# Performance work log

Measured on AMD Instinct MI355X. Metric: run time of the kernel, lower is better.

Reference implementation:

```python
import jax, jax.numpy as jnp
import numpy as np

VOCAB = 50000; D = 512; H = 512; HD = H // 2; L = 2
T = 2048; NTAGS = 20; START = 18; END = 19
NEG = -10000.0


def setup_inputs() -> dict:
    key = jax.random.key(0)
    ks = jax.random.split(key, 24)
    s = 0.05
    rn = lambda k, shape: jax.random.normal(k, shape, jnp.float32) * s
    inp = {}
    inp["sentence"] = jax.random.randint(ks[0], (T,), 0, VOCAB)
    inp["emb"] = rn(ks[1], (VOCAB, D))
    i = 2
    for l in range(L):
        din = D if l == 0 else H
        for d in ("f", "b"):
            inp[f"l{l}{d}_Wih"] = rn(ks[i], (4 * HD, din)); i += 1
            inp[f"l{l}{d}_Whh"] = rn(ks[i], (4 * HD, HD)); i += 1
            inp[f"l{l}{d}_bih"] = rn(ks[i], (4 * HD,)); i += 1
            inp[f"l{l}{d}_bhh"] = rn(ks[i], (4 * HD,)); i += 1
    inp["W_out"] = rn(ks[i], (NTAGS, H)); i += 1
    inp["b_out"] = rn(ks[i], (NTAGS,)); i += 1
    tr = jax.random.normal(ks[i], (NTAGS, NTAGS), jnp.float32)
    tr = tr.at[START, :].set(NEG).at[:, END].set(NEG)
    inp["transitions"] = tr
    return inp


def _lstm_dir(x, Wih, Whh, bih, bhh, reverse):
    # x: [T, din]; precompute input contribution to all 4 gates (i,f,g,o order).
    xg = x @ Wih.T + bih  # [T, 4*HD]
    h0 = jnp.zeros((Whh.shape[1],), x.dtype)

    def step(carry, xt):
        h, c = carry
        z = xt + h @ Whh.T + bhh
        i, f, g, o = jnp.split(z, 4)
        c = jax.nn.sigmoid(f) * c + jax.nn.sigmoid(i) * jnp.tanh(g)
        h = jax.nn.sigmoid(o) * jnp.tanh(c)
        return (h, c), h

    _, hs = jax.lax.scan(step, (h0, h0), xg, reverse=reverse)
    return hs  # [T, HD], outputs aligned with timesteps in both directions


def _feats(sentence, emb, layers, W_out, b_out):
    x = emb[sentence]  # [T, D]
    for (Wf, Uf, bf, cf, Wb, Ub, bb, cb) in layers:
        hf = _lstm_dir(x, Wf, Uf, bf, cf, False)
        hb = _lstm_dir(x, Wb, Ub, bb, cb, True)
        x = jnp.concatenate([hf, hb], axis=-1)  # [T, H]
    return x @ W_out.T + b_out  # [T, NTAGS]


def _viterbi(feats, transitions):
    v0 = jnp.full((NTAGS,), NEG, feats.dtype).at[START].set(0.0)

    def step(v, feat):
        scores = v[None, :] + transitions  # [next_tag, prev_tag]
        bp = jnp.argmax(scores, axis=1)
        v_new = jnp.max(scores, axis=1) + feat
        return v_new, bp

    v_last, bps = jax.lax.scan(step, v0, feats)  # bps: [T, NTAGS]
    terminal = v_last + transitions[END]
    best = jnp.argmax(terminal)
    score = terminal[best]

    def back(tag, bp):
        return bp[tag], tag  # emit tag at this timestep, move to its predecessor

    _, path = jax.lax.scan(back, best, bps, reverse=True)
    return score, path


def reference(sentence, emb, l0f_Wih, l0f_Whh, l0f_bih, l0f_bhh, l0b_Wih, l0b_Whh, l0b_bih, l0b_bhh, l1f_Wih, l1f_Whh, l1f_bih, l1f_bhh, l1b_Wih, l1b_Whh, l1b_bih, l1b_bhh, W_out, b_out, transitions):
    layers = [
        (l0f_Wih, l0f_Whh, l0f_bih, l0f_bhh, l0b_Wih, l0b_Whh, l0b_bih, l0b_bhh),
        (l1f_Wih, l1f_Whh, l1f_bih, l1f_bhh, l1b_Wih, l1b_Whh, l1b_bih, l1b_bhh),
    ]
    feats = _feats(sentence, emb, layers, W_out, b_out)
    return _viterbi(feats, transitions)
```

## Files before the change

kernel.cpp:

```cpp
#include <hip/hip_runtime.h>
#include <math.h>


#define T_LEN 2048
#define DMODEL 512
#define HD 256
#define NTAGS 20
#define START_TAG 18
#define END_TAG 19
#define NCAND 64

__device__ __forceinline__ float fsig(float x) {
  return 1.0f / (1.0f + __expf(-x));
}
__device__ __forceinline__ float ftanh(float x) {
  float xc = fminf(15.0f, fmaxf(-15.0f, x));
  float e = __expf(2.0f * xc);
  return (e - 1.0f) / (e + 1.0f);
}

__device__ __forceinline__ unsigned long long rd_l2(unsigned long long* p) {
  unsigned long long old;
  unsigned long long zero = 0;
  asm volatile("global_atomic_add_x2 %0, %1, %2, off sc0\n\ts_waitcnt vmcnt(0)"
               : "=&v"(old)
               : "v"(p), "v"(zero)
               : "memory");
  return old;
}
__device__ __forceinline__ void pub_l2(unsigned long long* p,
                                       unsigned long long v) {
  *(volatile unsigned long long*)p = v;
}

__global__ void embed_k(const int* __restrict__ sent,
                        const float* __restrict__ emb,
                        float* __restrict__ x0) {
  int t = blockIdx.x;
  int tid = threadIdx.x;
  int tok = sent[t];
  const float4* src = (const float4*)(emb + (size_t)tok * DMODEL);
  float4* dst = (float4*)(x0 + (size_t)t * DMODEL);
  dst[tid] = src[tid];
}

__global__ __launch_bounds__(256) void gemm_xg_k(
    const float* __restrict__ X,
    const float* __restrict__ Wf, const float* __restrict__ Wb,
    const float* __restrict__ bf, const float* __restrict__ bb,
    float* __restrict__ outf, float* __restrict__ outb) {
  int bx = blockIdx.x;
  int by = blockIdx.y;
  int dir = blockIdx.z;
  const float* W = dir ? Wb : Wf;
  const float* bias = dir ? bb : bf;
  float* out = dir ? outb : outf;

  __shared__ __align__(16) float Xs[16][132];
  __shared__ __align__(16) float Ws[16][132];

  int tid = threadIdx.x;
  int tx = tid & 15;
  int ty = tid >> 4;

  float acc[8][8];
#pragma unroll
  for (int i = 0; i < 8; i++)
#pragma unroll
    for (int j = 0; j < 8; j++) acc[i][j] = 0.0f;

  for (int kt = 0; kt < DMODEL / 16; kt++) {
    __syncthreads();
#pragma unroll
    for (int l = 0; l < 2; l++) {
      int fi = tid + l * 256;
      int row = fi >> 2;
      int kq = fi & 3;
      float4 xv = *(const float4*)(X + (size_t)(by * 128 + row) * DMODEL + kt * 16 + kq * 4);
      Xs[kq * 4 + 0][row] = xv.x;
      Xs[kq * 4 + 1][row] = xv.y;
      Xs[kq * 4 + 2][row] = xv.z;
      Xs[kq * 4 + 3][row] = xv.w;
      float4 wv = *(const float4*)(W + (size_t)(bx * 128 + row) * DMODEL + kt * 16 + kq * 4);
      Ws[kq * 4 + 0][row] = wv.x;
      Ws[kq * 4 + 1][row] = wv.y;
      Ws[kq * 4 + 2][row] = wv.z;
      Ws[kq * 4 + 3][row] = wv.w;
    }
    __syncthreads();
#pragma unroll
    for (int k = 0; k < 16; k++) {
      float4 a0 = *(const float4*)&Xs[k][ty * 4];
      float4 a1 = *(const float4*)&Xs[k][64 + ty * 4];
      float4 b0 = *(const float4*)&Ws[k][tx * 4];
      float4 b1 = *(const float4*)&Ws[k][64 + tx * 4];
      float a[8] = {a0.x, a0.y, a0.z, a0.w, a1.x, a1.y, a1.z, a1.w};
      float b[8] = {b0.x, b0.y, b0.z, b0.w, b1.x, b1.y, b1.z, b1.w};
#pragma unroll
      for (int i = 0; i < 8; i++)
#pragma unroll
        for (int j = 0; j < 8; j++) acc[i][j] += a[i] * b[j];
    }
  }

  float4 bv0 = *(const float4*)(bias + bx * 128 + tx * 4);
  float4 bv1 = *(const float4*)(bias + bx * 128 + 64 + tx * 4);
  float bb8[8] = {bv0.x, bv0.y, bv0.z, bv0.w, bv1.x, bv1.y, bv1.z, bv1.w};
#pragma unroll
  for (int i = 0; i < 8; i++) {
    int row = by * 128 + ((i < 4) ? (ty * 4 + i) : (64 + ty * 4 + (i - 4)));
    float4 o0 = {acc[i][0] + bb8[0], acc[i][1] + bb8[1], acc[i][2] + bb8[2], acc[i][3] + bb8[3]};
    float4 o1 = {acc[i][4] + bb8[4], acc[i][5] + bb8[5], acc[i][6] + bb8[6], acc[i][7] + bb8[7]};
    *(float4*)(out + (size_t)row * 1024 + bx * 128 + tx * 4) = o0;
    *(float4*)(out + (size_t)row * 1024 + bx * 128 + 64 + tx * 4) = o1;
  }
}

__attribute__((amdgpu_waves_per_eu(1, 1)))
__global__ __launch_bounds__(256) void recur_k(
    const float* __restrict__ xg_f, const float* __restrict__ xg_b,
    const float* __restrict__ Whh_f, const float* __restrict__ Whh_b,
    const float* __restrict__ bhh_f, const float* __restrict__ bhh_b,
    float* __restrict__ xnext, unsigned long long* __restrict__ hcomm_base,
    int* __restrict__ elect_base, unsigned long long* __restrict__ probe_base,
    int* __restrict__ vote_base) {
  int dir = blockIdx.y;
  int tid = threadIdx.x;

  int xcd;
  asm volatile("s_getreg_b32 %0, hwreg(HW_REG_XCC_ID)" : "=s"(xcd));
  xcd &= 7;
  int* cnt = elect_base + dir * (1 + NCAND);
  int* tab = cnt + 1;

  __shared__ int e_tab[NCAND];
  __shared__ int e_info[4];
  __shared__ int probe_ok[8];
  if (tid == 0) {
    int ticket = __hip_atomic_fetch_add(cnt, 1, __ATOMIC_RELAXED,
                                        __HIP_MEMORY_SCOPE_AGENT);
    __hip_atomic_store(&tab[ticket], xcd + 1, __ATOMIC_RELAXED,
                       __HIP_MEMORY_SCOPE_AGENT);
    e_info[0] = ticket;
  }
  if (tid < NCAND) {
    int v;
    do {
      v = __hip_atomic_load(&tab[tid], __ATOMIC_RELAXED,
                            __HIP_MEMORY_SCOPE_AGENT);
    } while (v == 0);
    e_tab[tid] = v - 1;
  }
  __syncthreads();
  if (tid == 0) {
    int ticket = e_info[0];
    int counts[8] = {0, 0, 0, 0, 0, 0, 0, 0};
    int home = -1;
    for (int i = 0; i < NCAND; i++) {
      int x = e_tab[i];
      counts[x]++;
      if (counts[x] == 8 && home < 0) home = x;
    }
    int sel = 0, kc = 0, probe = 0;
    if (home >= 0) {
      if (xcd == home) {
        int rank = 0;
        for (int i = 0; i < ticket; i++)
          if (e_tab[i] == home) rank++;
        if (rank < 8) { sel = 1; kc = rank; probe = 1; }
      }
    } else {
      if (ticket < 8) { sel = 1; kc = ticket; probe = 0; }
    }
    e_info[1] = sel; e_info[2] = kc; e_info[3] = probe;
  }
  __syncthreads();
  if (!e_info[1]) return;
  int kc = e_info[2];
  int do_probe = e_info[3];
  int use_l2 = 0;

  if (do_probe) {
    unsigned long long* probe = probe_base + (size_t)dir * 8 * 16;
    int* vote = vote_base + dir * 8;
    if (tid == 0) {
      pub_l2(&probe[kc * 16], 0xBEEF000000000000ull + (unsigned)kc);
    }
    if (tid < 8) {
      int found = 0;
      for (int iter = 0; iter < 3000 && !found; ++iter) {
        if (rd_l2(&probe[tid * 16]) ==
            0xBEEF000000000000ull + (unsigned)tid) found = 1;
      }
      probe_ok[tid] = found;
    }
    __syncthreads();
    if (tid == 0) {
      int ok = 1;
      for (int i = 0; i < 8; i++) ok &= probe_ok[i];
      __hip_atomic_store(&vote[kc], 1 + ok, __ATOMIC_RELAXED,
                         __HIP_MEMORY_SCOPE_AGENT);
    }
    if (tid < 8) {
      int v;
      do {
        v = __hip_atomic_load(&vote[tid], __ATOMIC_RELAXED,
                              __HIP_MEMORY_SCOPE_AGENT);
      } while (v == 0);
      probe_ok[tid] = v;
    }
    __syncthreads();
    if (tid == 0) {
      int all2 = 1;
      for (int i = 0; i < 8; i++) all2 &= (probe_ok[i] == 2);
      e_info[3] = all2;
    }
    __syncthreads();
    use_l2 = e_info[3];
  }

  const float* Whh = dir ? Whh_b : Whh_f;
  const float* bhh = dir ? bhh_b : bhh_f;
  const float* xg = dir ? xg_b : xg_f;
  unsigned long long* hcomm = hcomm_base + (size_t)dir * 2 * HD;

  int r = tid >> 1;
  int half = tid & 1;
  int g = r >> 5;
  int kl = r & 31;
  int grow = g * 256 + kc * 32 + kl;

  float4 Wv[32];
  const float4* wrow = (const float4*)(Whh + (size_t)grow * HD + half * 128);
#pragma unroll
  for (int j = 0; j < 32; j++) Wv[j] = wrow[j];
#pragma unroll
  for (int j = 0; j < 32; j++) {
    asm volatile("" : "+v"(Wv[j].x), "+v"(Wv[j].y), "+v"(Wv[j].z),
                      "+v"(Wv[j].w));
  }
  float bias = bhh[grow];

  __shared__ __align__(16) float hbuf[272];
  __shared__ float zbuf[128];
  hbuf[tid] = 0.0f;
  if (tid < 16) hbuf[256 + tid] = 0.0f;
  __syncthreads();

  float c = 0.0f;
  bool is_remote = ((tid >> 5) != kc);

  float xgv_next = 0.0f;
  {
    int t0 = dir ? (T_LEN - 1) : 0;
    if (!half) xgv_next = xg[(size_t)t0 * 1024 + grow];
  }

#pragma unroll 1
  for (int it = 0; it < T_LEN; ++it) {
    int t = dir ? (T_LEN - 1 - it) : it;
    int p = it & 1;
    unsigned int tag = (unsigned)(it + 1);

    float xgv = xgv_next;
    if (it + 1 < T_LEN) {
      int tn = dir ? (T_LEN - 2 - it) : (it + 1);
      if (!half) xgv_next = xg[(size_t)tn * 1024 + grow];
    }

    const float4* h4 = (const float4*)hbuf + half * 34;
    float4 acc = {0.f, 0.f, 0.f, 0.f};
#pragma unroll
    for (int j = 0; j < 32; j++) {
      float4 hv = h4[j];
      acc.x += Wv[j].x * hv.x;
      acc.y += Wv[j].y * hv.y;
      acc.z += Wv[j].z * hv.z;
      acc.w += Wv[j].w * hv.w;
    }
    float s = (acc.x + acc.y) + (acc.z + acc.w);
    s += __shfl_xor(s, 1, 64);
    if (!half) zbuf[r] = s + xgv + bias;
    __syncthreads();

    if (tid < 32) {
      float zi = zbuf[tid];
      float zf = zbuf[32 + tid];
      float zg = zbuf[64 + tid];
      float zo = zbuf[96 + tid];
      c = fsig(zf) * c + fsig(zi) * ftanh(zg);
      float h = fsig(zo) * ftanh(c);
      union { float f; unsigned u; } cv;
      cv.f = h;
      unsigned long long pkt = ((unsigned long long)tag << 32) | cv.u;
      int e = kc * 32 + tid;
      if (use_l2) {
        pub_l2(&hcomm[p * HD + e], pkt);
      } else {
        __hip_atomic_store(&hcomm[p * HD + e], pkt,
                           __ATOMIC_RELAXED, __HIP_MEMORY_SCOPE_AGENT);
      }
      xnext[(size_t)t * DMODEL + dir * HD + e] = h;
      hbuf[((e >> 7) * 136) + (e & 127)] = h;
    }
    if (is_remote) {
      unsigned long long v;
      if (use_l2) {
        do { v = rd_l2(&hcomm[p * HD + tid]); } while ((unsigned)(v >> 32) != tag);
      } else {
        do {
          v = __hip_atomic_load(&hcomm[p * HD + tid], __ATOMIC_RELAXED,
                                __HIP_MEMORY_SCOPE_AGENT);
        } while ((unsigned)(v >> 32) != tag);
      }
      union { unsigned u; float f; } cv;
      cv.u = (unsigned)v;
      hbuf[((tid >> 7) * 136) + (tid & 127)] = cv.f;
    }
    __syncthreads();
  }
}

__global__ void proj_k(const float* __restrict__ x2,
                       const float* __restrict__ Wo,
                       const float* __restrict__ bo,
                       float* __restrict__ feats) {
  int t = blockIdx.x;
  int tid = threadIdx.x;
  int n = tid & 31;
  int seg = tid >> 5;
  __shared__ float red[8][32];
  float s = 0.0f;
  if (n < NTAGS) {
    const float* xr = x2 + (size_t)t * DMODEL + seg * 64;
    const float* wr = Wo + (size_t)n * DMODEL + seg * 64;
#pragma unroll
    for (int j = 0; j < 64; j++) s += xr[j] * wr[j];
  }
  red[seg][n] = s;
  __syncthreads();
  if (tid < NTAGS) {
    float tot = bo[tid];
#pragma unroll
    for (int k = 0; k < 8; k++) tot += red[k][tid];
    feats[(size_t)t * NTAGS + tid] = tot;
  }
}

__global__ void viterbi_k(const float* __restrict__ feats,
                          const float* __restrict__ tr,
                          float* __restrict__ out) {
  __shared__ float v[NTAGS];
  __shared__ unsigned char bp[T_LEN * NTAGS];
  __shared__ float term[NTAGS];
  int tid = threadIdx.x;

  float trrow[NTAGS];
  if (tid < NTAGS) {
#pragma unroll
    for (int p = 0; p < NTAGS; p++) trrow[p] = tr[tid * NTAGS + p];
    v[tid] = (tid == START_TAG) ? 0.0f : -10000.0f;
  }
  __syncthreads();

#pragma unroll 1
  for (int t = 0; t < T_LEN; t++) {
    float fv = 0.0f;
    if (tid < NTAGS) fv = feats[(size_t)t * NTAGS + tid];
    float best = -3.4e38f;
    int arg = 0;
    if (tid < NTAGS) {
#pragma unroll
      for (int p = 0; p < NTAGS; p++) {
        float sc = v[p] + trrow[p];
        if (sc > best) { best = sc; arg = p; }
      }
      bp[t * NTAGS + tid] = (unsigned char)arg;
    }
    __syncthreads();
    if (tid < NTAGS) v[tid] = best + fv;
    __syncthreads();
  }

  if (tid < NTAGS) term[tid] = v[tid] + tr[END_TAG * NTAGS + tid];
  __syncthreads();
  if (tid == 0) {
    float bs = term[0];
    int bi = 0;
    for (int p = 1; p < NTAGS; p++) {
      if (term[p] > bs) { bs = term[p]; bi = p; }
    }
    out[0] = bs;
    int tag = bi;
    for (int t = T_LEN - 1; t >= 0; t--) {
      out[1 + t] = (float)tag;
      tag = bp[t * NTAGS + tag];
    }
  }
}

extern "C" void kernel_launch(void* const* d_in, const int* in_sizes, int n_in,
                              void* d_out, int out_size, void* d_ws, size_t ws_size,
                              hipStream_t stream) {
  const int* sent = (const int*)d_in[0];
  const float* emb = (const float*)d_in[1];
  const float* l0f_Wih = (const float*)d_in[2];
  const float* l0f_Whh = (const float*)d_in[3];
  const float* l0f_bih = (const float*)d_in[4];
  const float* l0f_bhh = (const float*)d_in[5];
  const float* l0b_Wih = (const float*)d_in[6];
  const float* l0b_Whh = (const float*)d_in[7];
  const float* l0b_bih = (const float*)d_in[8];
  const float* l0b_bhh = (const float*)d_in[9];
  const float* l1f_Wih = (const float*)d_in[10];
  const float* l1f_Whh = (const float*)d_in[11];
  const float* l1f_bih = (const float*)d_in[12];
  const float* l1f_bhh = (const float*)d_in[13];
  const float* l1b_Wih = (const float*)d_in[14];
  const float* l1b_Whh = (const float*)d_in[15];
  const float* l1b_bih = (const float*)d_in[16];
  const float* l1b_bhh = (const float*)d_in[17];
  const float* W_out = (const float*)d_in[18];
  const float* b_out = (const float*)d_in[19];
  const float* transitions = (const float*)d_in[20];

  char* ws = (char*)d_ws;
  size_t off = 0;
  float* x0 = (float*)(ws + off);  off += (size_t)T_LEN * DMODEL * 4;
  float* xgf = (float*)(ws + off); off += (size_t)T_LEN * 1024 * 4;
  float* xgb = (float*)(ws + off); off += (size_t)T_LEN * 1024 * 4;
  float* x1 = (float*)(ws + off);  off += (size_t)T_LEN * DMODEL * 4;
  float* x2 = (float*)(ws + off);  off += (size_t)T_LEN * DMODEL * 4;
  float* feats = (float*)(ws + off); off += (size_t)T_LEN * NTAGS * 4;

  off = (off + 127) & ~(size_t)127;
  char* sync_area = ws + off;
  unsigned long long* hcomm0 = (unsigned long long*)(sync_area);
  unsigned long long* hcomm1 = (unsigned long long*)(sync_area + 8192);
  int* elect0 = (int*)(sync_area + 16384);
  int* elect1 = (int*)(sync_area + 18432);
  unsigned long long* probe0 = (unsigned long long*)(sync_area + 20480);
  unsigned long long* probe1 = (unsigned long long*)(sync_area + 22528);
  int* vote0 = (int*)(sync_area + 24576);
  int* vote1 = (int*)(sync_area + 25600);
  size_t sync_bytes = 26624;
  off += sync_bytes;

  float* outf = (float*)d_out;

  (void)hipMemsetAsync(sync_area, 0, sync_bytes, stream);

  embed_k<<<dim3(T_LEN), dim3(128), 0, stream>>>(sent, emb, x0);

  gemm_xg_k<<<dim3(8, 16, 2), dim3(256), 0, stream>>>(
      x0, l0f_Wih, l0b_Wih, l0f_bih, l0b_bih, xgf, xgb);

  recur_k<<<dim3(NCAND, 2), dim3(256), 0, stream>>>(
      xgf, xgb, l0f_Whh, l0b_Whh, l0f_bhh, l0b_bhh, x1, hcomm0, elect0,
      probe0, vote0);

  gemm_xg_k<<<dim3(8, 16, 2), dim3(256), 0, stream>>>(
      x1, l1f_Wih, l1b_Wih, l1f_bih, l1b_bih, xgf, xgb);

  recur_k<<<dim3(NCAND, 2), dim3(256), 0, stream>>>(
      xgf, xgb, l1f_Whh, l1b_Whh, l1f_bhh, l1b_bhh, x2, hcomm1, elect1,
      probe1, vote1);

  proj_k<<<dim3(T_LEN), dim3(256), 0, stream>>>(x2, W_out, b_out, feats);

  viterbi_k<<<dim3(1), dim3(64), 0, stream>>>(feats, transitions, outf);
}
```

Measured before the change: 7.894 ms.

## Use per-chunk flag polling and a ring buffer for hidden-state exchange

In the recurrent kernel's L2 path, the double-buffered hidden-state mailbox becomes a 32-slot ring. Each producer chunk now publishes a single per-chunk flag after its data stores complete. Consumers spin on 8 flags, with 8 lanes polling via L2 atomics, and then read the ring slot with a plain volatile load, falling back to atomic polling only on a tag mismatch. The aim is to cut the number of threads spinning on L2 atomics each step, at the cost of an extra flag write, a store fence and an added dependency hop per timestep.

New measurement: 9.827 ms. 1.24x slower.

```diff
diff --git a/kernel.cpp b/kernel.cpp
--- a/kernel.cpp
+++ b/kernel.cpp
@@ -9,6 +9,7 @@
 #define START_TAG 18
 #define END_TAG 19
 #define NCAND 64
+#define RING 32
 
 __device__ __forceinline__ float fsig(float x) {
   return 1.0f / (1.0f + __expf(-x));
@@ -121,7 +122,10 @@
     const float* __restrict__ xg_f, const float* __restrict__ xg_b,
     const float* __restrict__ Whh_f, const float* __restrict__ Whh_b,
     const float* __restrict__ bhh_f, const float* __restrict__ bhh_b,
-    float* __restrict__ xnext, unsigned long long* __restrict__ hcomm_base,
+    float* __restrict__ xnext,
+    unsigned long long* __restrict__ hcomm_fb_base,
+    unsigned long long* __restrict__ ring_base,
+    unsigned long long* __restrict__ flags_base,
     int* __restrict__ elect_base, unsigned long long* __restrict__ probe_base,
     int* __restrict__ vote_base) {
   int dir = blockIdx.y;
@@ -222,7 +226,9 @@
   const float* Whh = dir ? Whh_b : Whh_f;
   const float* bhh = dir ? bhh_b : bhh_f;
   const float* xg = dir ? xg_b : xg_f;
-  unsigned long long* hcomm = hcomm_base + (size_t)dir * 2 * HD;
+  unsigned long long* hcomm_fb = hcomm_fb_base + (size_t)dir * 2 * HD;
+  unsigned long long* ring = ring_base + (size_t)dir * RING * HD;
+  unsigned long long* flags = flags_base + (size_t)dir * 64;
 
   int r = tid >> 1;
   int half = tid & 1;
@@ -261,6 +267,7 @@
     int t = dir ? (T_LEN - 1 - it) : it;
     int p = it & 1;
     unsigned int tag = (unsigned)(it + 1);
+    unsigned long long* rs = ring + (size_t)(it & (RING - 1)) * HD;
 
     float xgv = xgv_next;
     if (it + 1 < T_LEN) {
@@ -295,24 +302,42 @@
       unsigned long long pkt = ((unsigned long long)tag << 32) | cv.u;
       int e = kc * 32 + tid;
       if (use_l2) {
-        pub_l2(&hcomm[p * HD + e], pkt);
+        pub_l2(&rs[e], pkt);
+        asm volatile("s_waitcnt vmcnt(0)" ::: "memory");
+        if (tid == 0) pub_l2(&flags[kc * 8], (unsigned long long)tag);
       } else {
-        __hip_atomic_store(&hcomm[p * HD + e], pkt,
+        __hip_atomic_store(&hcomm_fb[p * HD + e], pkt,
                            __ATOMIC_RELAXED, __HIP_MEMORY_SCOPE_AGENT);
       }
       xnext[(size_t)t * DMODEL + dir * HD + e] = h;
       hbuf[((e >> 7) * 136) + (e & 127)] = h;
     }
-    if (is_remote) {
+
+    if (use_l2) {
+      int lane = tid & 63;
+      int wv = tid >> 6;
+      if (lane < 2) {
+        int ch = wv * 2 + lane;
+        if (ch != kc) {
+          unsigned long long fv;
+          do { fv = rd_l2(&flags[ch * 8]); } while (fv < (unsigned long long)tag);
+        }
+      }
+      if (is_remote) {
+        unsigned long long v = *(volatile unsigned long long*)&rs[tid];
+        if ((unsigned)(v >> 32) != tag) {
+          do { v = rd_l2(&rs[tid]); } while ((unsigned)(v >> 32) != tag);
+        }
+        union { unsigned u; float f; } cv;
+        cv.u = (unsigned)v;
+        hbuf[((tid >> 7) * 136) + (tid & 127)] = cv.f;
+      }
+    } else if (is_remote) {
       unsigned long long v;
-      if (use_l2) {
-        do { v = rd_l2(&hcomm[p * HD + tid]); } while ((unsigned)(v >> 32) != tag);
-      } else {
-        do {
-          v = __hip_atomic_load(&hcomm[p * HD + tid], __ATOMIC_RELAXED,
-                                __HIP_MEMORY_SCOPE_AGENT);
-        } while ((unsigned)(v >> 32) != tag);
-      }
+      do {
+        v = __hip_atomic_load(&hcomm_fb[p * HD + tid], __ATOMIC_RELAXED,
+                              __HIP_MEMORY_SCOPE_AGENT);
+      } while ((unsigned)(v >> 32) != tag);
       union { unsigned u; float f; } cv;
       cv.u = (unsigned)v;
       hbuf[((tid >> 7) * 136) + (tid & 127)] = cv.f;
@@ -435,15 +460,26 @@
 
   off = (off + 127) & ~(size_t)127;
   char* sync_area = ws + off;
-  unsigned long long* hcomm0 = (unsigned long long*)(sync_area);
-  unsigned long long* hcomm1 = (unsigned long long*)(sync_area + 8192);
-  int* elect0 = (int*)(sync_area + 16384);
-  int* elect1 = (int*)(sync_area + 18432);
-  unsigned long long* probe0 = (unsigned long long*)(sync_area + 20480);
-  unsigned long long* probe1 = (unsigned long long*)(sync_area + 22528);
-  int* vote0 = (int*)(sync_area + 24576);
-  int* vote1 = (int*)(sync_area + 25600);
-  size_t sync_bytes = 26624;
+  size_t fb_b = 2 * 2 * HD * 8;
+  size_t ring_b = 2 * (size_t)RING * HD * 8;
+  size_t flg_b = 2 * 64 * 8;
+  size_t layer_b = fb_b + ring_b + flg_b;
+  char* L0 = sync_area;
+  char* L1 = sync_area + layer_b;
+  unsigned long long* fb0 = (unsigned long long*)(L0);
+  unsigned long long* ring0 = (unsigned long long*)(L0 + fb_b);
+  unsigned long long* flg0 = (unsigned long long*)(L0 + fb_b + ring_b);
+  unsigned long long* fb1 = (unsigned long long*)(L1);
+  unsigned long long* ring1 = (unsigned long long*)(L1 + fb_b);
+  unsigned long long* flg1 = (unsigned long long*)(L1 + fb_b + ring_b);
+  char* aux = sync_area + 2 * layer_b;
+  int* elect0 = (int*)(aux);
+  int* elect1 = (int*)(aux + 2048);
+  unsigned long long* probe0 = (unsigned long long*)(aux + 4096);
+  unsigned long long* probe1 = (unsigned long long*)(aux + 6144);
+  int* vote0 = (int*)(aux + 8192);
+  int* vote1 = (int*)(aux + 9216);
+  size_t sync_bytes = 2 * layer_b + 10240;
   off += sync_bytes;
 
   float* outf = (float*)d_out;
@@ -456,15 +492,15 @@
       x0, l0f_Wih, l0b_Wih, l0f_bih, l0b_bih, xgf, xgb);
 
   recur_k<<<dim3(NCAND, 2), dim3(256), 0, stream>>>(
-      xgf, xgb, l0f_Whh, l0b_Whh, l0f_bhh, l0b_bhh, x1, hcomm0, elect0,
-      probe0, vote0);
+      xgf, xgb, l0f_Whh, l0b_Whh, l0f_bhh, l0b_bhh, x1, fb0, ring0, flg0,
+      elect0, probe0, vote0);
 
   gemm_xg_k<<<dim3(8, 16, 2), dim3(256), 0, stream>>>(
       x1, l1f_Wih, l1b_Wih, l1f_bih, l1b_bih, xgf, xgb);
 
   recur_k<<<dim3(NCAND, 2), dim3(256), 0, stream>>>(
-      xgf, xgb, l1f_Whh, l1b_Whh, l1f_bhh, l1b_bhh, x2, hcomm1, elect1,
-      probe1, vote1);
+      xgf, xgb, l1f_Whh, l1b_Whh, l1f_bhh, l1b_bhh, x2, fb1, ring1, flg1,
+      elect1, probe1, vote1);
 
   proj_k<<<dim3(T_LEN), dim3(256), 0, stream>>>(x2, W_out, b_out, feats);
 
```
